# Kernel tuning notes

Measured on AMD Instinct MI355X. Metric: run time of the kernel, lower is better.

## Reference

```python
import jax, jax.numpy as jnp
import numpy as np

B, T, H, S = 64, 512, 768, 128  # batch, seq_len, hidden_size, num_statements


def setup_inputs() -> dict:
    key = jax.random.key(0)
    ks = jax.random.split(key, 6)
    hidden = jax.random.normal(ks[0], (B, T, H), dtype=jnp.float32)
    # per-token statement ids, sorted (statements appear contiguously in source order)
    statements_ids = jnp.sort(jax.random.randint(ks[1], (B, T), 0, S), axis=-1).astype(jnp.int32)
    scale = 1.0 / np.sqrt(H)
    w1 = jax.random.normal(ks[2], (H, H), dtype=jnp.float32) * scale
    b1 = jnp.zeros((H,), dtype=jnp.float32)
    w2 = jax.random.normal(ks[3], (H, H), dtype=jnp.float32) * scale
    b2 = jnp.zeros((H,), dtype=jnp.float32)
    w3 = jax.random.normal(ks[4], (H, 1), dtype=jnp.float32) * scale
    b3 = jnp.zeros((1,), dtype=jnp.float32)
    return {"hidden": hidden, "statements_ids": statements_ids,
            "w1": w1, "b1": b1, "w2": w2, "b2": b2, "w3": w3, "b3": b3}


def _segment_mean(x, sid):
    # x: [T, H], sid: [T] -> [S, H] mean of tokens per statement id
    sums = jax.ops.segment_sum(x, sid, num_segments=S)            # [S, H]
    cnts = jax.ops.segment_sum(jnp.ones((x.shape[0],), x.dtype), sid, num_segments=S)  # [S]
    return sums / jnp.maximum(cnts, 1.0)[:, None]


def reference(hidden, statements_ids, w1, b1, w2, b2, w3, b3):
    # per-statement mean pooling (scatter-mean), vectorized over batch
    pooled = jax.vmap(_segment_mean)(hidden, statements_ids)      # [B, S, H]
    # CodeCoverageMLP: fc1 -> GELU -> fc2 -> GELU -> fc3 -> sigmoid (dropout = eval identity)
    x = jax.nn.gelu(pooled @ w1 + b1, approximate=False)
    x = jax.nn.gelu(x @ w2 + b2, approximate=False)
    preds = jax.nn.sigmoid(x @ w3 + b3)                           # [B, S, 1]
    return preds[..., 0]                                          # [B, S]
```

## Files before the change

kernel.cpp:

```cpp
#include <hip/hip_runtime.h>
#include <stdint.h>

#define NB 64
#define NT 512
#define NH 768
#define NS 128
#define NM (NB*NS)

typedef _Float16 half8 __attribute__((ext_vector_type(8)));
typedef _Float16 half4 __attribute__((ext_vector_type(4)));
typedef __attribute__((ext_vector_type(4))) float f32x4;

__device__ __forceinline__ float gelu_fast(float x) {
  float ax = fabsf(x) * 0.70710678118654752440f;
  float t  = __builtin_amdgcn_rcpf(1.0f + 0.3275911f * ax);
  float e  = __expf(-ax * ax);
  float poly = t * (0.254829592f + t * (-0.284496736f +
               t * (1.421413741f + t * (-1.453152027f + t * 1.061405429f))));
  float erfv = 1.0f - poly * e;
  float phi  = 0.5f * (1.0f + copysignf(erfv, x));
  return x * phi;
}

__device__ __forceinline__ void gll16(const void* g, void* l) {
  __builtin_amdgcn_global_load_lds(
      (__attribute__((address_space(1))) unsigned int*)g,
      (__attribute__((address_space(3))) unsigned int*)l,
      16, 0, 0);
}

__global__ void prep_w_kernel(const float* __restrict__ w1, const float* __restrict__ w2,
                              _Float16* __restrict__ W) {
  int id = blockIdx.x * 256 + threadIdx.x;
  int n  = id % NH;
  int t  = id / NH;
  int kc = t % 96;
  int w  = t / 96;
  const float* src = w ? w2 : w1;
  int k0 = kc * 8;
  half8 h;
#pragma unroll
  for (int i = 0; i < 8; ++i)
    h[i] = (_Float16)src[(size_t)(k0 + i) * NH + n];
  const size_t off = ((((size_t)w * 48 + (n >> 4)) * 96 + kc) * 16 + (n & 15)) * 8;
  *(half8*)&W[off] = h;
}

__global__ __launch_bounds__(256)
void pool_kernel(const float* __restrict__ hidden, const int* __restrict__ sid,
                 _Float16* __restrict__ Ahi, _Float16* __restrict__ Alo) {
  __shared__ int   s_sid[NT];
  __shared__ short s_e0[NS + 1];
  const int b = blockIdx.y, cc = blockIdx.x;
  const int tid = threadIdx.x;
  for (int t = tid; t < NT; t += 256) s_sid[t] = sid[b * NT + t];
  __syncthreads();
  for (int t = tid; t < NT; t += 256) {
    const int cur  = s_sid[t];
    const int prev = t ? s_sid[t - 1] : -1;
    for (int s = prev + 1; s <= cur; ++s) s_e0[s] = (short)t;
    if (t == NT - 1)
      for (int s = cur + 1; s <= NS; ++s) s_e0[s] = (short)NT;
  }
  __syncthreads();

  const int c4  = tid & 15;
  const int sg  = tid >> 4;
  const int col = cc * 64 + c4 * 4;
  const float* hb = hidden + (size_t)b * NT * NH;

  for (int s = sg; s < NS; s += 16) {
    const int e0 = s_e0[s], e1 = s_e0[s + 1];
    f32x4 acc = {0.f, 0.f, 0.f, 0.f};
    for (int t = e0; t < e1; ++t)
      acc += *(const f32x4*)(hb + (size_t)t * NH + col);
    const float inv = 1.0f / (float)((e1 > e0) ? (e1 - e0) : 1);
    const int m = b * NS + s;
    half4 h, l;
#pragma unroll
    for (int j = 0; j < 4; ++j) {
      float x = acc[j] * inv;
      h[j] = (_Float16)x;
      l[j] = (_Float16)(x - (float)h[j]);
    }
    const size_t off = (size_t)m * NH + col;
    *(half4*)&Ahi[off] = h;
    *(half4*)&Alo[off] = l;
  }
}

__global__ __launch_bounds__(512, 4)
void mlp_kernel(const _Float16* __restrict__ Ahi, const _Float16* __restrict__ Alo,
                const _Float16* __restrict__ Wp,
                const float* __restrict__ b1, const float* __restrict__ b2,
                const float* __restrict__ w3, const float* __restrict__ b3,
                float* __restrict__ out) {
  __shared__ _Float16 sA[2][4096];
  __shared__ _Float16 sX[32 * NH];
  float (*sP)[32] = (float(*)[32])&sA[0][0];

  const int tid  = threadIdx.x;
  const int lane = tid & 63;
  const int wv   = tid >> 6;
  const int lr   = lane & 15;
  const int lk4  = lane >> 4;
  const int row0 = blockIdx.x * 32;

  const _Float16* W1 = Wp;
  const _Float16* W2 = Wp + (size_t)NH * NH;

  const int str  = wv * 4 + lk4;
  const int scol = (lr * 8) ^ ((str & 7) << 3);
#define STAGE(kt) {                                                           \
    const size_t src = (size_t)(row0 + str) * NH + (kt) * 128 + scol;         \
    gll16(Ahi + src, &sA[0][wv * 512]);                                       \
    gll16(Alo + src, &sA[1][wv * 512]); }

  f32x4 acc1[2][6] = {};
  STAGE(0);
  __syncthreads();
  for (int kt = 0; kt < 6; ++kt) {
    half8 bw[6], bwn[6];
#pragma unroll
    for (int nf = 0; nf < 6; ++nf)
      bw[nf] = *(const half8*)(W1 + ((size_t)(wv * 6 + nf) * 96 + kt * 16 + lk4) * 128 + lr * 8);
#pragma unroll
    for (int kk = 0; kk < 4; ++kk) {
      if (kk < 3) {
#pragma unroll
        for (int nf = 0; nf < 6; ++nf)
          bwn[nf] = *(const half8*)(W1 + ((size_t)(wv * 6 + nf) * 96 + kt * 16 + (kk + 1) * 4 + lk4) * 128 + lr * 8);
      }
#pragma unroll
      for (int mf = 0; mf < 2; ++mf) {
        const int ar = mf * 16 + lr;
        const int ad = ar * 128 + ((kk * 32 + lk4 * 8) ^ ((ar & 7) << 3));
        half8 ah = *(const half8*)&sA[0][ad];
        half8 al = *(const half8*)&sA[1][ad];
#pragma unroll
        for (int nf = 0; nf < 6; ++nf) {
          acc1[mf][nf] = __builtin_amdgcn_mfma_f32_16x16x32_f16(ah, bw[nf], acc1[mf][nf], 0, 0, 0);
          acc1[mf][nf] = __builtin_amdgcn_mfma_f32_16x16x32_f16(al, bw[nf], acc1[mf][nf], 0, 0, 0);
        }
      }
#pragma unroll
      for (int nf = 0; nf < 6; ++nf) bw[nf] = bwn[nf];
    }
    __syncthreads();
    if (kt < 5) {
      STAGE(kt + 1);
      __syncthreads();
    }
  }

#pragma unroll
  for (int nf = 0; nf < 6; ++nf) {
    const int col = wv * 96 + nf * 16 + lr;
    const float bv = b1[col];
#pragma unroll
    for (int mf = 0; mf < 2; ++mf)
#pragma unroll
      for (int r = 0; r < 4; ++r) {
        const int row = mf * 16 + lk4 * 4 + r;
        sX[row * NH + (col ^ ((row & 7) << 3))] = (_Float16)gelu_fast(acc1[mf][nf][r] + bv);
      }
  }
  __syncthreads();

  f32x4 acc2[2][6] = {};
  half8 bw2[6], bw2n[6];
#pragma unroll
  for (int nf = 0; nf < 6; ++nf)
    bw2[nf] = *(const half8*)(W2 + ((size_t)(wv * 6 + nf) * 96 + lk4) * 128 + lr * 8);
  for (int g = 0; g < 24; ++g) {
    if (g < 23) {
#pragma unroll
      for (int nf = 0; nf < 6; ++nf)
        bw2n[nf] = *(const half8*)(W2 + ((size_t)(wv * 6 + nf) * 96 + (g + 1) * 4 + lk4) * 128 + lr * 8);
    }
    const int koff = g * 32 + lk4 * 8;
#pragma unroll
    for (int mf = 0; mf < 2; ++mf) {
      const int ar = mf * 16 + lr;
      half8 a = *(const half8*)&sX[ar * NH + (koff ^ ((ar & 7) << 3))];
#pragma unroll
      for (int nf = 0; nf < 6; ++nf)
        acc2[mf][nf] = __builtin_amdgcn_mfma_f32_16x16x32_f16(a, bw2[nf], acc2[mf][nf], 0, 0, 0);
    }
#pragma unroll
    for (int nf = 0; nf < 6; ++nf) bw2[nf] = bw2n[nf];
  }

  float p[2][4] = {};
#pragma unroll
  for (int nf = 0; nf < 6; ++nf) {
    const int col = wv * 96 + nf * 16 + lr;
    const float bv = b2[col], wvv = w3[col];
#pragma unroll
    for (int mf = 0; mf < 2; ++mf)
#pragma unroll
      for (int r = 0; r < 4; ++r)
        p[mf][r] += gelu_fast(acc2[mf][nf][r] + bv) * wvv;
  }
#pragma unroll
  for (int mf = 0; mf < 2; ++mf)
#pragma unroll
    for (int r = 0; r < 4; ++r) {
      float v = p[mf][r];
      v += __shfl_xor(v, 1, 16);
      v += __shfl_xor(v, 2, 16);
      v += __shfl_xor(v, 4, 16);
      v += __shfl_xor(v, 8, 16);
      if (lr == 0) sP[wv][mf * 16 + lk4 * 4 + r] = v;
    }
  __syncthreads();
  if (tid < 32) {
    float s = b3[0];
#pragma unroll
    for (int w = 0; w < 8; ++w) s += sP[w][tid];
    out[row0 + tid] = 1.0f / (1.0f + expf(-s));
  }
#undef STAGE
}

extern "C" void kernel_launch(void* const* d_in, const int* in_sizes, int n_in,
                              void* d_out, int out_size, void* d_ws, size_t ws_size,
                              hipStream_t stream) {
  (void)in_sizes; (void)n_in; (void)out_size; (void)ws_size;
  const float* hidden = (const float*)d_in[0];
  const int*   sid    = (const int*)d_in[1];
  const float* w1     = (const float*)d_in[2];
  const float* b1     = (const float*)d_in[3];
  const float* w2     = (const float*)d_in[4];
  const float* b2     = (const float*)d_in[5];
  const float* w3     = (const float*)d_in[6];
  const float* b3     = (const float*)d_in[7];
  float* out = (float*)d_out;

  char* p = (char*)d_ws;
  const size_t actE = (size_t)NM * NH;
  _Float16* Ahi = (_Float16*)p; p += actE * 2;
  _Float16* Alo = (_Float16*)p; p += actE * 2;
  _Float16* W   = (_Float16*)p; p += (size_t)2 * NH * NH * 2;

  prep_w_kernel<<<2 * 96 * NH / 256, 256, 0, stream>>>(w1, w2, W);
  pool_kernel<<<dim3(12, NB), 256, 0, stream>>>(hidden, sid, Ahi, Alo);
  mlp_kernel<<<NM / 32, 512, 0, stream>>>(Ahi, Alo, W, b1, b2, w3, b3, out);
}
```

Measured before the change: 227.1 us.

## Repartition pooling by statement groups with full-row coalesced loads and prefetch

The pooling kernel now gives each block a group of 8 statements and all 768 columns, instead of a 64-column slice covering all statements. Each thread streams tokens across the group's contiguous token range, prefetches the next row, and flushes segment sums into a shared-memory accumulator before normalizing and writing the hi/lo fp16 outputs. The goal is fully coalesced row reads and better load balance. The cost is a serial token loop per thread, a 24KB shared buffer, and uneven work when groups differ in token count.

```diff
diff --git a/kernel.cpp b/kernel.cpp
--- a/kernel.cpp
+++ b/kernel.cpp
@@ -46,44 +46,66 @@
   *(half8*)&W[off] = h;
 }
 
-__global__ __launch_bounds__(256)
+__global__ __launch_bounds__(192)
 void pool_kernel(const float* __restrict__ hidden, const int* __restrict__ sid,
                  _Float16* __restrict__ Ahi, _Float16* __restrict__ Alo) {
   __shared__ int   s_sid[NT];
   __shared__ short s_e0[NS + 1];
-  const int b = blockIdx.y, cc = blockIdx.x;
+  __shared__ float sAcc[8][NH];
+  const int b = blockIdx.y, g = blockIdx.x;
   const int tid = threadIdx.x;
-  for (int t = tid; t < NT; t += 256) s_sid[t] = sid[b * NT + t];
-  __syncthreads();
-  for (int t = tid; t < NT; t += 256) {
+
+  for (int t = tid; t < NT; t += 192) s_sid[t] = sid[b * NT + t];
+  __syncthreads();
+  for (int t = tid; t < NT; t += 192) {
     const int cur  = s_sid[t];
     const int prev = t ? s_sid[t - 1] : -1;
     for (int s = prev + 1; s <= cur; ++s) s_e0[s] = (short)t;
     if (t == NT - 1)
       for (int s = cur + 1; s <= NS; ++s) s_e0[s] = (short)NT;
   }
-  __syncthreads();
-
-  const int c4  = tid & 15;
-  const int sg  = tid >> 4;
-  const int col = cc * 64 + c4 * 4;
+#pragma unroll
+  for (int i = 0; i < 8; ++i)
+    *(f32x4*)&sAcc[0][(i * 192 + tid) * 4] = (f32x4){0.f, 0.f, 0.f, 0.f};
+  __syncthreads();
+
+  const int s0 = g * 8;
+  const int t0 = s_e0[s0], t1 = s_e0[s0 + 8];
+  const int col = tid * 4;
   const float* hb = hidden + (size_t)b * NT * NH;
 
-  for (int s = sg; s < NS; s += 16) {
-    const int e0 = s_e0[s], e1 = s_e0[s + 1];
-    f32x4 acc = {0.f, 0.f, 0.f, 0.f};
-    for (int t = e0; t < e1; ++t)
-      acc += *(const f32x4*)(hb + (size_t)t * NH + col);
-    const float inv = 1.0f / (float)((e1 > e0) ? (e1 - e0) : 1);
-    const int m = b * NS + s;
+  f32x4 acc = {0.f, 0.f, 0.f, 0.f};
+  int cur = (t0 < t1) ? s_sid[t0] : -1;
+  f32x4 nxt;
+  if (t0 < t1) nxt = *(const f32x4*)(hb + (size_t)t0 * NH + col);
+  for (int t = t0; t < t1; ++t) {
+    f32x4 v = nxt;
+    if (t + 1 < t1) nxt = *(const f32x4*)(hb + (size_t)(t + 1) * NH + col);
+    const int s = s_sid[t];
+    if (s != cur) {
+      *(f32x4*)&sAcc[cur - s0][col] = acc;
+      acc = (f32x4){0.f, 0.f, 0.f, 0.f};
+      cur = s;
+    }
+    acc += v;
+  }
+  if (cur >= 0) *(f32x4*)&sAcc[cur - s0][col] = acc;
+  __syncthreads();
+
+#pragma unroll
+  for (int s = 0; s < 8; ++s) {
+    const int gs = s0 + s;
+    const int cnt = s_e0[gs + 1] - s_e0[gs];
+    const float inv = 1.0f / (float)(cnt > 0 ? cnt : 1);
+    f32x4 v = *(const f32x4*)&sAcc[s][col];
     half4 h, l;
 #pragma unroll
     for (int j = 0; j < 4; ++j) {
-      float x = acc[j] * inv;
+      float x = v[j] * inv;
       h[j] = (_Float16)x;
       l[j] = (_Float16)(x - (float)h[j]);
     }
-    const size_t off = (size_t)m * NH + col;
+    const size_t off = (size_t)(b * NS + gs) * NH + col;
     *(half4*)&Ahi[off] = h;
     *(half4*)&Alo[off] = l;
   }
@@ -244,6 +266,6 @@
   _Float16* W   = (_Float16*)p; p += (size_t)2 * NH * NH * 2;
 
   prep_w_kernel<<<2 * 96 * NH / 256, 256, 0, stream>>>(w1, w2, W);
-  pool_kernel<<<dim3(12, NB), 256, 0, stream>>>(hidden, sid, Ahi, Alo);
+  pool_kernel<<<dim3(16, NB), 192, 0, stream>>>(hidden, sid, Ahi, Alo);
   mlp_kernel<<<NM / 32, 512, 0, stream>>>(Ahi, Alo, W, b1, b2, w3, b3, out);
 }
```

New measurement: 226.1 us. No clear change (-0.4%).
